# Kernel tuning notes

Measured on AMD Instinct MI355X. Metric: run time of the kernel, lower is better.

Reference implementation:

```python
import jax, jax.numpy as jnp
import numpy as np

N_NODES = 50000
N_EDGES = 1500000
D = 512
LN_EPS = 1e-5


def setup_inputs() -> dict:
    key = jax.random.key(0)
    ks = jax.random.split(key, 8)
    scale = 1.0 / np.sqrt(D)
    return {
        "node_feature": jax.random.normal(ks[0], (N_NODES, D), dtype=jnp.float32),
        "edge_index": jax.random.randint(ks[1], (2, N_EDGES), 0, N_NODES, dtype=jnp.int32),
        "W_l": jax.random.uniform(ks[2], (D, D), jnp.float32, -scale, scale),  # neighbor lin
        "b_l": jnp.zeros((D,), jnp.float32),
        "W_r": jax.random.uniform(ks[3], (D, D), jnp.float32, -scale, scale),  # root lin (no bias)
        "gamma": jnp.ones((D,), jnp.float32),
        "beta": jnp.zeros((D,), jnp.float32),
    }


def _layer_norm(x, gamma, beta):
    mu = jnp.mean(x, axis=-1, keepdims=True)
    var = jnp.mean(jnp.square(x - mu), axis=-1, keepdims=True)
    return (x - mu) * jax.lax.rsqrt(var + LN_EPS) * gamma + beta


def reference(node_feature, edge_index, W_l, b_l, W_r, gamma, beta):
    n = node_feature.shape[0]
    residual = node_feature
    h = _layer_norm(node_feature, gamma, beta)
    src, dst = edge_index[0], edge_index[1]
    # mean-aggregate source features at destinations (gather + segment scatter)
    summed = jax.ops.segment_sum(h[src], dst, num_segments=n)  # [N, D]
    cnt = jax.ops.segment_sum(jnp.ones((src.shape[0],), h.dtype), dst, num_segments=n)
    mean = summed / jnp.maximum(cnt, 1.0)[:, None]
    # SAGEConv: lin_l(aggregated) + lin_r(root); bias on lin_l
    out = mean @ W_l.T + b_l + h @ W_r.T
    out = jax.nn.relu(out)
    return out + residual
```

## Files before the change

kernel.cpp:

```cpp
#include <hip/hip_runtime.h>


#define D_DIM 512

typedef __bf16 bf16x8 __attribute__((ext_vector_type(8)));
typedef float f32x4 __attribute__((ext_vector_type(4)));
typedef float f32x2 __attribute__((ext_vector_type(2)));

__device__ __forceinline__ unsigned short f2bf(float f) {
  unsigned u = __float_as_uint(f);
  u += 0x7fffu + ((u >> 16) & 1u);
  return (unsigned short)(u >> 16);
}
__device__ __forceinline__ float bflo(unsigned u) { return __uint_as_float(u << 16); }
__device__ __forceinline__ float bfhi(unsigned u) { return __uint_as_float(u & 0xffff0000u); }
__device__ __forceinline__ unsigned packbf2(float lo, float hi) {
  return (unsigned)f2bf(lo) | ((unsigned)f2bf(hi) << 16);
}

__global__ void ln_kernel(const float* __restrict__ x, const float* __restrict__ gamma,
                          const float* __restrict__ beta, unsigned short* __restrict__ Acat,
                          unsigned char* __restrict__ h8, int n, int use_fp8) {
  int lane = threadIdx.x & 63;
  int row = blockIdx.x * 4 + (threadIdx.x >> 6);
  if (row >= n) return;
  const float* xr = x + (size_t)row * D_DIM + lane * 8;
  float4 a = *(const float4*)xr;
  float4 b = *(const float4*)(xr + 4);
  float sum = a.x + a.y + a.z + a.w + b.x + b.y + b.z + b.w;
  float sq = a.x * a.x + a.y * a.y + a.z * a.z + a.w * a.w +
             b.x * b.x + b.y * b.y + b.z * b.z + b.w * b.w;
#pragma unroll
  for (int m = 1; m < 64; m <<= 1) {
    sum += __shfl_xor(sum, m, 64);
    sq  += __shfl_xor(sq, m, 64);
  }
  float mu = sum * (1.0f / D_DIM);
  float var = sq * (1.0f / D_DIM) - mu * mu;
  float rs = rsqrtf(var + 1e-5f);
  const float* gp = gamma + lane * 8;
  const float* bp = beta + lane * 8;
  float4 g0 = *(const float4*)gp, g1 = *(const float4*)(gp + 4);
  float4 e0 = *(const float4*)bp, e1 = *(const float4*)(bp + 4);
  float h0 = (a.x - mu) * rs * g0.x + e0.x;
  float h1 = (a.y - mu) * rs * g0.y + e0.y;
  float h2 = (a.z - mu) * rs * g0.z + e0.z;
  float h3 = (a.w - mu) * rs * g0.w + e0.w;
  float h4 = (b.x - mu) * rs * g1.x + e1.x;
  float h5 = (b.y - mu) * rs * g1.y + e1.y;
  float h6 = (b.z - mu) * rs * g1.z + e1.z;
  float h7 = (b.w - mu) * rs * g1.w + e1.w;
  uint4 st = { packbf2(h0, h1), packbf2(h2, h3), packbf2(h4, h5), packbf2(h6, h7) };
  *(uint4*)(Acat + (size_t)row * 1024 + 512 + lane * 8) = st;
  if (use_fp8) {
    int p0 = __builtin_amdgcn_cvt_pk_fp8_f32(h0, h1, 0, false);
    p0 = __builtin_amdgcn_cvt_pk_fp8_f32(h2, h3, p0, true);
    int p1 = __builtin_amdgcn_cvt_pk_fp8_f32(h4, h5, 0, false);
    p1 = __builtin_amdgcn_cvt_pk_fp8_f32(h6, h7, p1, true);
    uint2 st2 = { (unsigned)p0, (unsigned)p1 };
    *(uint2*)(h8 + (size_t)row * 512 + lane * 8) = st2;
  }
}

__global__ void wconv_kernel(const float* __restrict__ Wl, const float* __restrict__ Wr,
                             unsigned short* __restrict__ Wcat) {
  int id = blockIdx.x * 256 + threadIdx.x;
  int j = id >> 9, k = id & 511;
  Wcat[(size_t)j * 1024 + k] = f2bf(Wl[id]);
  Wcat[(size_t)j * 1024 + 512 + k] = f2bf(Wr[id]);
}

__global__ void zero_kernel(int* __restrict__ p, int n) {
  int i = blockIdx.x * 256 + threadIdx.x;
  if (i < n) p[i] = 0;
}

__global__ void hist_kernel(const int* __restrict__ dst, int nE, int* __restrict__ cnt) {
  int e = blockIdx.x * 256 + threadIdx.x;
  if (e < nE) atomicAdd(&cnt[dst[e]], 1);
}

__global__ void scan1_kernel(const int* __restrict__ cnt, int n,
                             int* __restrict__ excl, int* __restrict__ bsums) {
  __shared__ int wsum[16];
  int gid = blockIdx.x * 1024 + threadIdx.x;
  int lane = threadIdx.x & 63, wave = threadIdx.x >> 6;
  int v = (gid < n) ? cnt[gid] : 0;
  int s = v;
#pragma unroll
  for (int d = 1; d < 64; d <<= 1) {
    int t = __shfl_up(s, d, 64);
    if (lane >= d) s += t;
  }
  if (lane == 63) wsum[wave] = s;
  __syncthreads();
  if (wave == 0) {
    int ws = (lane < 16) ? wsum[lane] : 0;
#pragma unroll
    for (int d = 1; d < 16; d <<= 1) {
      int t = __shfl_up(ws, d, 64);
      if (lane >= d) ws += t;
    }
    if (lane < 16) wsum[lane] = ws;
  }
  __syncthreads();
  int incl = s + ((wave > 0) ? wsum[wave - 1] : 0);
  if (gid < n) excl[gid] = incl - v;
  if (threadIdx.x == 1023) bsums[blockIdx.x] = incl;
}

__global__ void scan2_kernel(int* __restrict__ bsums, int nb) {
  int lane = threadIdx.x;
  int v = (lane < nb) ? bsums[lane] : 0;
  int s = v;
#pragma unroll
  for (int d = 1; d < 64; d <<= 1) {
    int t = __shfl_up(s, d, 64);
    if (lane >= d) s += t;
  }
  if (lane < nb) bsums[lane] = s - v;
}

__global__ void scan3_kernel(int* __restrict__ rowst, int* __restrict__ cur,
                             const int* __restrict__ bsums, int n, int nE) {
  int gid = blockIdx.x * 1024 + threadIdx.x;
  if (gid < n) {
    int r = rowst[gid] + bsums[blockIdx.x];
    rowst[gid] = r;
    cur[gid] = r;
  }
  if (gid == 0) rowst[n] = nE;
}

__global__ void scatter_kernel(const int* __restrict__ src, const int* __restrict__ dst,
                               int nE, int* __restrict__ cur, int* __restrict__ sorted_src) {
  int e = blockIdx.x * 256 + threadIdx.x;
  if (e < nE) {
    int p = atomicAdd(&cur[dst[e]], 1);
    sorted_src[p] = src[e];
  }
}

__device__ __forceinline__ void acc_bf(float* acc, uint4 r) {
  acc[0] += bflo(r.x); acc[1] += bfhi(r.x);
  acc[2] += bflo(r.y); acc[3] += bfhi(r.y);
  acc[4] += bflo(r.z); acc[5] += bfhi(r.z);
  acc[6] += bflo(r.w); acc[7] += bfhi(r.w);
}

__device__ __forceinline__ void acc_f8(float* acc, uint2 r) {
  f32x2 a = __builtin_amdgcn_cvt_pk_f32_fp8(r.x, false);
  f32x2 b = __builtin_amdgcn_cvt_pk_f32_fp8(r.x, true);
  f32x2 c = __builtin_amdgcn_cvt_pk_f32_fp8(r.y, false);
  f32x2 d = __builtin_amdgcn_cvt_pk_f32_fp8(r.y, true);
  acc[0] += a.x; acc[1] += a.y; acc[2] += b.x; acc[3] += b.y;
  acc[4] += c.x; acc[5] += c.y; acc[6] += d.x; acc[7] += d.y;
}

__global__ void agg_kernel(unsigned short* __restrict__ Acat,
                           const unsigned char* __restrict__ h8,
                           const int* __restrict__ rowst,
                           const int* __restrict__ sorted_src, int n, int use_fp8) {
  int lane = threadIdx.x & 63;
  int node = blockIdx.x * 4 + (threadIdx.x >> 6);
  if (node >= n) return;
  int s0 = rowst[node], s1 = rowst[node + 1];
  float acc[8] = {0.f, 0.f, 0.f, 0.f, 0.f, 0.f, 0.f, 0.f};
  if (use_fp8) {
    const unsigned char* hb = h8 + lane * 8;
    int e = s0;
    for (; e + 3 < s1; e += 4) {
      int i0 = sorted_src[e], i1 = sorted_src[e + 1];
      int i2 = sorted_src[e + 2], i3 = sorted_src[e + 3];
      uint2 r0 = *(const uint2*)(hb + (size_t)i0 * 512);
      uint2 r1 = *(const uint2*)(hb + (size_t)i1 * 512);
      uint2 r2 = *(const uint2*)(hb + (size_t)i2 * 512);
      uint2 r3 = *(const uint2*)(hb + (size_t)i3 * 512);
      acc_f8(acc, r0); acc_f8(acc, r1); acc_f8(acc, r2); acc_f8(acc, r3);
    }
    for (; e < s1; ++e) {
      uint2 r0 = *(const uint2*)(hb + (size_t)sorted_src[e] * 512);
      acc_f8(acc, r0);
    }
  } else {
    const unsigned short* hbase = Acat + 512 + lane * 8;
    int e = s0;
    for (; e + 3 < s1; e += 4) {
      int i0 = sorted_src[e], i1 = sorted_src[e + 1];
      int i2 = sorted_src[e + 2], i3 = sorted_src[e + 3];
      uint4 r0 = *(const uint4*)(hbase + (size_t)i0 * 1024);
      uint4 r1 = *(const uint4*)(hbase + (size_t)i1 * 1024);
      uint4 r2 = *(const uint4*)(hbase + (size_t)i2 * 1024);
      uint4 r3 = *(const uint4*)(hbase + (size_t)i3 * 1024);
      acc_bf(acc, r0); acc_bf(acc, r1); acc_bf(acc, r2); acc_bf(acc, r3);
    }
    for (; e < s1; ++e) {
      uint4 r0 = *(const uint4*)(hbase + (size_t)sorted_src[e] * 1024);
      acc_bf(acc, r0);
    }
  }
  int deg = s1 - s0;
  float sc = (deg > 0) ? (1.0f / (float)deg) : 0.0f;
  uint4 st = { packbf2(acc[0] * sc, acc[1] * sc), packbf2(acc[2] * sc, acc[3] * sc),
               packbf2(acc[4] * sc, acc[5] * sc), packbf2(acc[6] * sc, acc[7] * sc) };
  *(uint4*)(Acat + (size_t)node * 1024 + lane * 8) = st;
}

__device__ __forceinline__ void async16(const unsigned short* g, char* lds) {
  __builtin_amdgcn_global_load_lds((const __attribute__((address_space(1))) void*)g,
                                   (__attribute__((address_space(3))) void*)lds, 16, 0, 0);
}

__global__ __launch_bounds__(512, 2) void gemm_kernel(
    const unsigned short* __restrict__ A,
    const unsigned short* __restrict__ B,
    const float* __restrict__ bias,
    const float* __restrict__ residual,
    float* __restrict__ out, int M, int Mtiles) {
  __shared__ unsigned short sA[2][256 * 64];
  __shared__ unsigned short sB[2][128 * 64];
  const int K = 1024;
  int t = threadIdx.x;
  int lane = t & 63, wave = t >> 6;
  int quad = lane >> 4, l16 = lane & 15;
  int b = blockIdx.x;
  int mb = (b >> 5) * 8 + (b & 7);
  int nb = (b >> 3) & 3;
  if (mb >= Mtiles) return;
  int mBase = mb * 256, nBase = nb * 128;
  int wm = (wave >> 1) * 64;
  int wn = (wave & 1) * 64;

  int srow = t >> 3;
  int schunk = ((t & 7) ^ ((t >> 3) & 7)) * 8;
  const unsigned short* gAb = A + (size_t)(mBase + srow) * K + schunk;
  const unsigned short* gBb = B + (size_t)(nBase + srow) * K + schunk;

  f32x4 acc[4][4] = {};

  auto stage = [&](int buf, int kt) {
    int kOff = kt << 6;
    char* la = (char*)&sA[buf][0] + wave * 1024;
    char* lb = (char*)&sB[buf][0] + wave * 1024;
#pragma unroll
    for (int ia = 0; ia < 4; ++ia)
      async16(gAb + (size_t)ia * 64 * K + kOff, la + ia * 8192);
#pragma unroll
    for (int ib = 0; ib < 2; ++ib)
      async16(gBb + (size_t)ib * 64 * K + kOff, lb + ib * 8192);
  };

  int swz = (l16 & 7);
  auto compute = [&](int buf) {
    const unsigned short* pA = &sA[buf][0];
    const unsigned short* pB = &sB[buf][0];
#pragma unroll
    for (int kk = 0; kk < 2; ++kk) {
      bf16x8 af[4], bfr[4];
#pragma unroll
      for (int i = 0; i < 4; ++i) {
        int rr = wm + i * 16 + l16;
        int pc = (kk * 4 + quad) ^ swz;
        af[i] = *(const bf16x8*)(pA + rr * 64 + pc * 8);
      }
#pragma unroll
      for (int j = 0; j < 4; ++j) {
        int rb = wn + j * 16 + l16;
        int pc = (kk * 4 + quad) ^ swz;
        bfr[j] = *(const bf16x8*)(pB + rb * 64 + pc * 8);
      }
      __builtin_amdgcn_s_setprio(1);
#pragma unroll
      for (int i = 0; i < 4; ++i)
#pragma unroll
        for (int j = 0; j < 4; ++j)
          acc[i][j] = __builtin_amdgcn_mfma_f32_16x16x32_bf16(af[i], bfr[j], acc[i][j], 0, 0, 0);
      __builtin_amdgcn_s_setprio(0);
    }
  };

  stage(0, 0);
  asm volatile("s_waitcnt vmcnt(0)\n\ts_barrier" ::: "memory");
  for (int kt = 0; kt < 15; ++kt) {
    stage((kt + 1) & 1, kt + 1);
    compute(kt & 1);
    asm volatile("s_waitcnt vmcnt(0)\n\ts_barrier" ::: "memory");
  }
  compute(1);

  float biasv[4];
#pragma unroll
  for (int j = 0; j < 4; ++j) biasv[j] = bias[nBase + wn + j * 16 + l16];
#pragma unroll
  for (int i = 0; i < 4; ++i) {
    int gr0 = mBase + wm + i * 16 + quad * 4;
#pragma unroll
    for (int j = 0; j < 4; ++j) {
      int col = nBase + wn + j * 16 + l16;
#pragma unroll
      for (int r = 0; r < 4; ++r) {
        int gr = gr0 + r;
        if (gr < M) {
          size_t idx = (size_t)gr * D_DIM + col;
          float v = acc[i][j][r] + biasv[j];
          float rv = __builtin_nontemporal_load(&residual[idx]);
          __builtin_nontemporal_store(fmaxf(v, 0.0f) + rv, &out[idx]);
        }
      }
    }
  }
}

extern "C" void kernel_launch(void* const* d_in, const int* in_sizes, int n_in,
                              void* d_out, int out_size, void* d_ws, size_t ws_size,
                              hipStream_t stream) {
  const float* x = (const float*)d_in[0];
  const int* ei = (const int*)d_in[1];
  const float* Wl = (const float*)d_in[2];
  const float* bl = (const float*)d_in[3];
  const float* Wr = (const float*)d_in[4];
  const float* gamma = (const float*)d_in[5];
  const float* beta = (const float*)d_in[6];
  float* out = (float*)d_out;

  int n = in_sizes[0] / D_DIM;
  int nE = in_sizes[1] / 2;
  const int* src = ei;
  const int* dstv = ei + nE;
  int Mpad = (n + 255) & ~255;
  int Mtiles = Mpad / 256;

  char* w = (char*)d_ws;
  size_t off = 0;
  auto carve = [&](size_t bytes) {
    char* p = w + off;
    off += (bytes + 255) & ~(size_t)255;
    return p;
  };
  unsigned short* Acat = (unsigned short*)carve((size_t)Mpad * 1024 * 2);
  unsigned short* Wcat = (unsigned short*)carve((size_t)512 * 1024 * 2);
  int* sorted = (int*)carve((size_t)nE * 4);
  int* cnt = (int*)carve((size_t)n * 4);
  int* rowst = (int*)carve((size_t)(n + 1) * 4);
  int* bsums = (int*)carve(1024);
  if (off > ws_size) return;

  size_t h8_bytes = (size_t)n * 512;
  int use_fp8 = (off + h8_bytes <= ws_size) ? 1 : 0;
  unsigned char* h8 = use_fp8 ? (unsigned char*)carve(h8_bytes) : (unsigned char*)w;

  int nbScan = (n + 1023) / 1024;

  ln_kernel<<<(n + 3) / 4, 256, 0, stream>>>(x, gamma, beta, Acat, h8, n, use_fp8);
  wconv_kernel<<<(512 * 512) / 256, 256, 0, stream>>>(Wl, Wr, Wcat);
  zero_kernel<<<(n + 255) / 256, 256, 0, stream>>>(cnt, n);
  hist_kernel<<<(nE + 255) / 256, 256, 0, stream>>>(dstv, nE, cnt);
  scan1_kernel<<<nbScan, 1024, 0, stream>>>(cnt, n, rowst, bsums);
  scan2_kernel<<<1, 64, 0, stream>>>(bsums, nbScan);
  scan3_kernel<<<nbScan, 1024, 0, stream>>>(rowst, cnt, bsums, n, nE);
  scatter_kernel<<<(nE + 255) / 256, 256, 0, stream>>>(src, dstv, nE, cnt, sorted);
  agg_kernel<<<(n + 3) / 4, 256, 0, stream>>>(Acat, h8, rowst, sorted, n, use_fp8);
  int gemmBlocks = ((Mtiles + 7) / 8) * 32;
  gemm_kernel<<<gemmBlocks, 512, 0, stream>>>(Acat, Wcat, bl, x, out, n, Mtiles);
}
```

Measured before the change: 670.6 us.

## Keep full-K weight slice resident in LDS and stream A directly to registers

The GEMM now loads a 64-column slice of the concatenated weight matrix across the full K=1024 (128 KB) into LDS once. Each wave then streams its own 64 rows of A straight from global memory into registers, double-buffered across k-steps, instead of staging A and B tiles through LDS with per-step barriers. The block tile changes to 512x64 with 8 column blocks, and the padding and grid are adjusted to match. This drops the per-iteration barriers and LDS traffic for A. In exchange, occupancy is limited by the large LDS allocation, and A loads are exposed global latency with reuse only inside a wave.

```diff
diff --git a/kernel.cpp b/kernel.cpp
--- a/kernel.cpp
+++ b/kernel.cpp
@@ -217,86 +217,87 @@
     const float* __restrict__ bias,
     const float* __restrict__ residual,
     float* __restrict__ out, int M, int Mtiles) {
-  __shared__ unsigned short sA[2][256 * 64];
-  __shared__ unsigned short sB[2][128 * 64];
+  __shared__ unsigned short sB[64 * 1024];
   const int K = 1024;
   int t = threadIdx.x;
-  int lane = t & 63, wave = t >> 6;
+  int lane = t & 63, wv = t >> 6;
   int quad = lane >> 4, l16 = lane & 15;
   int b = blockIdx.x;
-  int mb = (b >> 5) * 8 + (b & 7);
-  int nb = (b >> 3) & 3;
+  int mb = (b >> 6) * 8 + (b & 7);
+  int nb = (b >> 3) & 7;
   if (mb >= Mtiles) return;
-  int mBase = mb * 256, nBase = nb * 128;
-  int wm = (wave >> 1) * 64;
-  int wn = (wave & 1) * 64;
-
-  int srow = t >> 3;
-  int schunk = ((t & 7) ^ ((t >> 3) & 7)) * 8;
-  const unsigned short* gAb = A + (size_t)(mBase + srow) * K + schunk;
-  const unsigned short* gBb = B + (size_t)(nBase + srow) * K + schunk;
-
+  int mBase = mb * 512, nBase = nb * 64;
+
+  {
+    char* ldsBase = (char*)&sB[0] + wv * 16384;
+    const unsigned short* gB = B + (size_t)(nBase + wv * 8) * K;
+#pragma unroll
+    for (int i = 0; i < 16; ++i) {
+      int s = (i >> 1) & 7;
+      const unsigned short* g = gB + (size_t)(i >> 1) * K + (i & 1) * 512 + ((lane ^ s) * 8);
+      async16(g, ldsBase + i * 1024);
+    }
+  }
+  asm volatile("s_waitcnt vmcnt(0)\n\ts_barrier" ::: "memory");
+
+  const unsigned short* gA = A + (size_t)(mBase + wv * 64 + l16) * K + quad * 8;
   f32x4 acc[4][4] = {};
-
-  auto stage = [&](int buf, int kt) {
-    int kOff = kt << 6;
-    char* la = (char*)&sA[buf][0] + wave * 1024;
-    char* lb = (char*)&sB[buf][0] + wave * 1024;
-#pragma unroll
-    for (int ia = 0; ia < 4; ++ia)
-      async16(gAb + (size_t)ia * 64 * K + kOff, la + ia * 8192);
-#pragma unroll
-    for (int ib = 0; ib < 2; ++ib)
-      async16(gBb + (size_t)ib * 64 * K + kOff, lb + ib * 8192);
-  };
-
-  int swz = (l16 & 7);
-  auto compute = [&](int buf) {
-    const unsigned short* pA = &sA[buf][0];
-    const unsigned short* pB = &sB[buf][0];
-#pragma unroll
-    for (int kk = 0; kk < 2; ++kk) {
-      bf16x8 af[4], bfr[4];
-#pragma unroll
-      for (int i = 0; i < 4; ++i) {
-        int rr = wm + i * 16 + l16;
-        int pc = (kk * 4 + quad) ^ swz;
-        af[i] = *(const bf16x8*)(pA + rr * 64 + pc * 8);
-      }
-#pragma unroll
-      for (int j = 0; j < 4; ++j) {
-        int rb = wn + j * 16 + l16;
-        int pc = (kk * 4 + quad) ^ swz;
-        bfr[j] = *(const bf16x8*)(pB + rb * 64 + pc * 8);
-      }
-      __builtin_amdgcn_s_setprio(1);
+  int swz = l16 & 7;
+
+  bf16x8 a0[4], a1[4];
+#pragma unroll
+  for (int i = 0; i < 4; ++i) a0[i] = *(const bf16x8*)(gA + (size_t)i * 16 * K);
+#pragma unroll
+  for (int i = 0; i < 4; ++i) a1[i] = *(const bf16x8*)(gA + (size_t)i * 16 * K + 32);
+
+  for (int kt = 0; kt < 32; kt += 2) {
+    bf16x8 bfr[4];
+#pragma unroll
+    for (int j = 0; j < 4; ++j) {
+      int pc = (kt * 4 + quad) ^ swz;
+      bfr[j] = *(const bf16x8*)(&sB[(j * 16 + l16) * 1024 + pc * 8]);
+    }
+    __builtin_amdgcn_s_setprio(1);
+#pragma unroll
+    for (int i = 0; i < 4; ++i)
+#pragma unroll
+      for (int j = 0; j < 4; ++j)
+        acc[i][j] = __builtin_amdgcn_mfma_f32_16x16x32_bf16(a0[i], bfr[j], acc[i][j], 0, 0, 0);
+    __builtin_amdgcn_s_setprio(0);
+    if (kt + 2 < 32) {
 #pragma unroll
       for (int i = 0; i < 4; ++i)
-#pragma unroll
-        for (int j = 0; j < 4; ++j)
-          acc[i][j] = __builtin_amdgcn_mfma_f32_16x16x32_bf16(af[i], bfr[j], acc[i][j], 0, 0, 0);
-      __builtin_amdgcn_s_setprio(0);
-    }
-  };
-
-  stage(0, 0);
-  asm volatile("s_waitcnt vmcnt(0)\n\ts_barrier" ::: "memory");
-  for (int kt = 0; kt < 15; ++kt) {
-    stage((kt + 1) & 1, kt + 1);
-    compute(kt & 1);
-    asm volatile("s_waitcnt vmcnt(0)\n\ts_barrier" ::: "memory");
-  }
-  compute(1);
+        a0[i] = *(const bf16x8*)(gA + (size_t)i * 16 * K + (kt + 2) * 32);
+    }
+    bf16x8 bfr2[4];
+#pragma unroll
+    for (int j = 0; j < 4; ++j) {
+      int pc = ((kt + 1) * 4 + quad) ^ swz;
+      bfr2[j] = *(const bf16x8*)(&sB[(j * 16 + l16) * 1024 + pc * 8]);
+    }
+    __builtin_amdgcn_s_setprio(1);
+#pragma unroll
+    for (int i = 0; i < 4; ++i)
+#pragma unroll
+      for (int j = 0; j < 4; ++j)
+        acc[i][j] = __builtin_amdgcn_mfma_f32_16x16x32_bf16(a1[i], bfr2[j], acc[i][j], 0, 0, 0);
+    __builtin_amdgcn_s_setprio(0);
+    if (kt + 3 < 32) {
+#pragma unroll
+      for (int i = 0; i < 4; ++i)
+        a1[i] = *(const bf16x8*)(gA + (size_t)i * 16 * K + (kt + 3) * 32);
+    }
+  }
 
   float biasv[4];
 #pragma unroll
-  for (int j = 0; j < 4; ++j) biasv[j] = bias[nBase + wn + j * 16 + l16];
+  for (int j = 0; j < 4; ++j) biasv[j] = bias[nBase + j * 16 + l16];
 #pragma unroll
   for (int i = 0; i < 4; ++i) {
-    int gr0 = mBase + wm + i * 16 + quad * 4;
+    int gr0 = mBase + wv * 64 + i * 16 + quad * 4;
 #pragma unroll
     for (int j = 0; j < 4; ++j) {
-      int col = nBase + wn + j * 16 + l16;
+      int col = nBase + j * 16 + l16;
 #pragma unroll
       for (int r = 0; r < 4; ++r) {
         int gr = gr0 + r;
@@ -327,8 +328,8 @@
   int nE = in_sizes[1] / 2;
   const int* src = ei;
   const int* dstv = ei + nE;
-  int Mpad = (n + 255) & ~255;
-  int Mtiles = Mpad / 256;
+  int Mpad = (n + 511) & ~511;
+  int Mtiles = Mpad / 512;
 
   char* w = (char*)d_ws;
   size_t off = 0;
@@ -360,6 +361,6 @@
   scan3_kernel<<<nbScan, 1024, 0, stream>>>(rowst, cnt, bsums, n, nE);
   scatter_kernel<<<(nE + 255) / 256, 256, 0, stream>>>(src, dstv, nE, cnt, sorted);
   agg_kernel<<<(n + 3) / 4, 256, 0, stream>>>(Acat, h8, rowst, sorted, n, use_fp8);
-  int gemmBlocks = ((Mtiles + 7) / 8) * 32;
+  int gemmBlocks = ((Mtiles + 7) / 8) * 64;
   gemm_kernel<<<gemmBlocks, 512, 0, stream>>>(Acat, Wcat, bl, x, out, n, Mtiles);
 }
```

After: 726.1 us. +8.3%, slower.
